# Performance work log

Hardware: AMD Instinct MI355X
Metric: run time of the kernel (lower is better)

## Reference

```python
import jax, jax.numpy as jnp
import numpy as np

N = 50000   # nodes
D = 256     # embed_dim
H = 256     # hidden_dim
E = 250000  # edges per relation type
T = 3       # edge types
NEG_SLOPE = 0.2  # PyG GATConv default


def setup_inputs() -> dict:
    key = jax.random.key(0)
    ks = jax.random.split(key, 12)
    s = lambda k, shape: jax.random.normal(k, shape, jnp.float32) * 0.05
    z = jax.random.normal(ks[0], (N, D), jnp.float32)
    ei = jax.random.randint(ks[1], (T, 2, E), 0, N, dtype=jnp.int32)
    W1 = s(ks[2], (T, D, H)); as1 = s(ks[3], (T, H)); ad1 = s(ks[4], (T, H))
    b1 = jnp.zeros((T, H), jnp.float32)
    W2 = s(ks[5], (T, H, H)); as2 = s(ks[6], (T, H)); ad2 = s(ks[7], (T, H))
    b2 = jnp.zeros((T, H), jnp.float32)
    Wh = s(ks[8], (H, 1)); bh = jnp.zeros((1,), jnp.float32)
    return dict(z=z, ei=ei, W1=W1, as1=as1, ad1=ad1, b1=b1,
                W2=W2, as2=as2, ad2=ad2, b2=b2, Wh=Wh, bh=bh)


def gat_conv(x, ei, W, a_s, a_d, b):
    # PyG GATConv, heads=1, no self loops: h = x W; e_ij = leaky_relu(a_s.h_j + a_d.h_i)
    # alpha = softmax over incoming edges of node i; out_i = sum_j alpha_ij h_j + bias
    src, dst = ei[0], ei[1]
    n = x.shape[0]
    h = x @ W                              # [N, H]
    a_src = h @ a_s                        # [N]
    a_dst = h @ a_d                        # [N]
    e = jax.nn.leaky_relu(a_src[src] + a_dst[dst], NEG_SLOPE)   # [E]
    m = jax.ops.segment_max(e, dst, num_segments=n)             # per-dst max
    ex = jnp.exp(e - m[dst])
    den = jax.ops.segment_sum(ex, dst, num_segments=n)
    alpha = ex / den[dst]                                       # [E]
    out = jax.ops.segment_sum(h[src] * alpha[:, None], dst, num_segments=n)
    return out + b


def layer(x, ei, W, a_s, a_d, b):
    # sum of per-type GATConv outputs, then ReLU (matches module)
    outs = jax.vmap(lambda e_, W_, s_, d_, b_: gat_conv(x, e_, W_, s_, d_, b_))(ei, W, a_s, a_d, b)
    return jax.nn.relu(outs.sum(0))


def reference(z, ei, W1, as1, ad1, b1, W2, as2, ad2, b2, Wh, bh):
    h1 = layer(z, ei, W1, as1, ad1, b1)
    h2 = layer(h1, ei, W2, as2, ad2, b2)
    return jax.nn.sigmoid(h2 @ Wh + bh).squeeze(-1)   # [N]
```

## Files before the change

### kernel.cpp

```cpp
#include <hip/hip_runtime.h>

#define GAT_N 50000
#define GAT_D 256
#define GAT_T 3
#define GAT_E 250000
#define GAT_B (GAT_T*GAT_N)
#define GAT_TOTE (GAT_T*GAT_E)
#define GAT_COLS (GAT_T*GAT_D)
#define GAT_SLOPE 0.2f

typedef unsigned short u16;
typedef unsigned int u32;
typedef __attribute__((ext_vector_type(8))) short s16x8;
typedef __attribute__((ext_vector_type(8))) __bf16 bf16x8;
typedef __attribute__((ext_vector_type(4))) float f32x4;
typedef __attribute__((ext_vector_type(2))) u32 u32x2;

__device__ __forceinline__ u16 f2bf(float f) {
    u32 x = __builtin_bit_cast(u32, f);
    u32 r = (x + 0x7fffu + ((x >> 16) & 1u)) >> 16;
    return (u16)r;
}
__device__ __forceinline__ float lo16(u32 w) {
    return __builtin_bit_cast(float, w << 16);
}
__device__ __forceinline__ float hi16(u32 w) {
    return __builtin_bit_cast(float, w & 0xffff0000u);
}

template<int CTRL>
__device__ __forceinline__ float dppadd(float x) {
    int y = __builtin_amdgcn_update_dpp(0, __builtin_bit_cast(int, x),
                                        CTRL, 0xf, 0xf, true);
    return x + __builtin_bit_cast(float, y);
}
__device__ __forceinline__ float sum16(float x) {
    x = dppadd<0xB1>(x);
    x = dppadd<0x4E>(x);
    x = dppadd<0x141>(x);
    x = dppadd<0x140>(x);
    return x;
}

__global__ void gat_prep(const float* __restrict__ W1, const float* __restrict__ W2,
                         const float* __restrict__ z, const float* __restrict__ b1,
                         const float* __restrict__ b2, const int* __restrict__ ei,
                         u16* __restrict__ WT1b, u16* __restrict__ WT2b,
                         u16* __restrict__ zb, u32* __restrict__ deg,
                         int* __restrict__ psrc2, float* __restrict__ bias3)
{
    int idx = blockIdx.x * 256 + threadIdx.x;
    if (idx < GAT_T * GAT_D * GAT_D) {
        int t = idx >> 16, r = idx & 65535;
        int h = r >> 8, d = r & 255;
        WT1b[idx] = f2bf(W1[t * 65536 + d * 256 + h]);
        WT2b[idx] = f2bf(W2[t * 65536 + d * 256 + h]);
    }
    if (idx < 2 * GAT_D) {
        const float* bb = (idx < GAT_D) ? b1 : b2;
        int c = idx & 255;
        bias3[idx] = bb[c] + bb[GAT_D + c] + bb[2 * GAT_D + c];
    }
    if (idx < GAT_TOTE) {
        int t = idx / GAT_E;
        int e = idx - t * GAT_E;
        int src = ei[t * 2 * GAT_E + e];
        int dst = ei[t * 2 * GAT_E + GAT_E + e];
        u32 slot = atomicAdd(&deg[dst], 1u);
        if (slot < 64u)
            psrc2[(size_t)dst * 64 + slot] = t * GAT_N + src;
    }
    if (idx < GAT_N * GAT_D / 4) {
        f32x4 v = ((const f32x4*)z)[idx];
        ushort4 pk;
        pk.x = f2bf(v.x); pk.y = f2bf(v.y); pk.z = f2bf(v.z); pk.w = f2bf(v.w);
        ((ushort4*)zb)[idx] = pk;
    }
}

__global__ __launch_bounds__(512, 4) void gat_gemm(
    const u16* __restrict__ A, const u16* __restrict__ WTb,
    u16* __restrict__ H, const float* __restrict__ as_in,
    const float* __restrict__ ad_in, float* __restrict__ a_s,
    float* __restrict__ a_d)
{
    int lin = blockIdx.x;
    int g   = lin / 48;
    int rem = lin - g * 48;
    int bc  = rem >> 3;
    int br  = (g << 3) + (rem & 7);
    if (br >= 391) return;

    __shared__ u16 Als[2][128 * 64];
    __shared__ u16 Bls[2][128 * 64];
    int tid  = threadIdx.x;
    int wave = tid >> 6, lane = tid & 63;
    int quad = lane >> 4, l16 = lane & 15;
    int wm = wave & 1, wn = wave >> 1;
    int lrow = lane >> 3;
    int swz  = ((lane & 7) ^ lrow) * 8;

    size_t arow0 = (size_t)br * 128;
    size_t brow0 = (size_t)bc * 128;

    auto STAGE = [&](int buf, int ks) {
        int k0 = ks * 64;
        #pragma unroll
        for (int r = 0; r < 2; ++r) {
            int srow = wave * 16 + r * 8 + lrow;
            const u16* gA = A   + (arow0 + srow) * GAT_D + k0 + swz;
            const u16* gB = WTb + (brow0 + srow) * GAT_D + k0 + swz;
            u16* lA = &Als[buf][wave * 1024 + r * 512];
            u16* lB = &Bls[buf][wave * 1024 + r * 512];
#if defined(__has_builtin) && __has_builtin(__builtin_amdgcn_global_load_lds)
            __builtin_amdgcn_global_load_lds(
                (const __attribute__((address_space(1))) void*)gA,
                (__attribute__((address_space(3))) void*)lA, 16, 0, 0);
            __builtin_amdgcn_global_load_lds(
                (const __attribute__((address_space(1))) void*)gB,
                (__attribute__((address_space(3))) void*)lB, 16, 0, 0);
#else
            *(s16x8*)(lA + lane * 8) = *(const s16x8*)gA;
            *(s16x8*)(lB + lane * 8) = *(const s16x8*)gB;
#endif
        }
    };

    f32x4 acc[4][2] = {};

    STAGE(0, 0);
    #pragma unroll
    for (int ks = 0; ks < 4; ++ks) {
        int cur = ks & 1;
        if (ks < 3) {
            STAGE(cur ^ 1, ks + 1);
            asm volatile("s_waitcnt vmcnt(4)" ::: "memory");
        } else {
            asm volatile("s_waitcnt vmcnt(0)" ::: "memory");
        }
        __builtin_amdgcn_s_barrier();

        #pragma unroll
        for (int kk = 0; kk < 2; ++kk) {
            int csw8 = ((kk * 4 + quad) ^ (l16 & 7)) * 8;
            bf16x8 af[4], bf[2];
            #pragma unroll
            for (int i = 0; i < 4; ++i)
                af[i] = __builtin_bit_cast(bf16x8,
                    *(const s16x8*)(&Als[cur][(wm * 64 + i * 16 + l16) * 64 + csw8]));
            #pragma unroll
            for (int j = 0; j < 2; ++j)
                bf[j] = __builtin_bit_cast(bf16x8,
                    *(const s16x8*)(&Bls[cur][(wn * 32 + j * 16 + l16) * 64 + csw8]));
            #pragma unroll
            for (int i = 0; i < 4; ++i)
                #pragma unroll
                for (int j = 0; j < 2; ++j)
                    acc[i][j] = __builtin_amdgcn_mfma_f32_16x16x32_bf16(
                        af[i], bf[j], acc[i][j], 0, 0, 0);
        }
        if (ks < 3)
            __builtin_amdgcn_s_barrier();
    }

    int gcol0 = bc * 128 + wn * 32;
    int t   = gcol0 >> 8;
    int ch0 = gcol0 & 255;
    u16* Ht = H + (size_t)t * GAT_N * GAT_D;
    int rowb = br * 128 + wm * 64 + quad * 4;
    #pragma unroll
    for (int i = 0; i < 4; ++i) {
        #pragma unroll
        for (int j = 0; j < 2; ++j) {
            int ch = ch0 + j * 16 + l16;
            #pragma unroll
            for (int r = 0; r < 4; ++r) {
                int row = rowb + i * 16 + r;
                if (row < GAT_N) Ht[(size_t)row * GAT_D + ch] = f2bf(acc[i][j][r]);
            }
        }
    }

    float asv[2], adv[2];
    #pragma unroll
    for (int j = 0; j < 2; ++j) {
        int ch = ch0 + j * 16 + l16;
        asv[j] = as_in[t * GAT_D + ch];
        adv[j] = ad_in[t * GAT_D + ch];
    }
    #pragma unroll
    for (int i = 0; i < 4; ++i) {
        float ps[4] = {}, pd[4] = {};
        #pragma unroll
        for (int j = 0; j < 2; ++j) {
            f32x4 a = acc[i][j];
            #pragma unroll
            for (int r = 0; r < 4; ++r) {
                ps[r] += a[r] * asv[j];
                pd[r] += a[r] * adv[j];
            }
        }
        #pragma unroll
        for (int r = 0; r < 4; ++r) {
            ps[r] = sum16(ps[r]);
            pd[r] = sum16(pd[r]);
        }
        if (l16 == 0) {
            int row = rowb + i * 16;
            #pragma unroll
            for (int r = 0; r < 4; ++r) {
                if (row + r < GAT_N) {
                    atomicAdd(&a_s[t * GAT_N + row + r], ps[r]);
                    atomicAdd(&a_d[t * GAT_N + row + r], pd[r]);
                }
            }
        }
    }
}

__global__ __launch_bounds__(64) void gat_gather(
    const u32* __restrict__ deg, const int* __restrict__ psrc2,
    const float* __restrict__ a_src, const float* __restrict__ a_dst,
    const u16* __restrict__ Hfb, const float* __restrict__ bias3,
    const float* __restrict__ Wh, const float* __restrict__ bh,
    int layer, u16* __restrict__ x2b, float* __restrict__ out)
{
    int n = blockIdx.x;
    int lane = threadIdx.x;

    u32 dv = deg[n];
    int dtot = (dv > 64u) ? 64 : (int)dv;

    int  j     = lane;
    bool valid = j < dtot;
    int  rs    = valid ? psrc2[(size_t)n * 64 + j] : 0;
    int  tj    = (rs >= GAT_N) + (rs >= 2 * GAT_N);

    float as   = a_src[rs];
    float adn  = a_dst[tj * GAT_N + n];

    const u16* Hl = Hfb + lane * 4;
    u32x2 w[8];
    #pragma unroll
    for (int u = 0; u < 8; ++u) {
        int rv = __builtin_amdgcn_readlane(rs, u);
        w[u] = *(const u32x2*)(Hl + (size_t)rv * GAT_D);
    }

    float e = as + adn;
    e = (e > 0.f) ? e : GAT_SLOPE * e;
    float ex = valid ? __expf(e) : 0.f;

    float s0 = (tj == 0) ? ex : 0.f;
    float s1 = (tj == 1) ? ex : 0.f;
    float s2 = (tj == 2) ? ex : 0.f;
    s0 = sum16(s0); s1 = sum16(s1); s2 = sum16(s2);
    #pragma unroll
    for (int d = 16; d < 64; d <<= 1) {
        s0 += __shfl_xor(s0, d);
        s1 += __shfl_xor(s1, d);
        s2 += __shfl_xor(s2, d);
    }
    float den = (tj == 0) ? s0 : ((tj == 1) ? s1 : s2);
    float alv = valid ? ex / den : 0.f;
    int av = __builtin_bit_cast(int, alv);

    float r[4] = {};
    int dpad = (dtot + 7) & ~7;
    for (int k0 = 0; ; k0 += 8) {
        float al[8]; u32x2 wc[8];
        #pragma unroll
        for (int u = 0; u < 8; ++u) {
            wc[u] = w[u];
            al[u] = __builtin_bit_cast(float,
                        __builtin_amdgcn_readlane(av, k0 + u));
        }
        bool more = (k0 + 8 < dpad);
        if (more) {
            #pragma unroll
            for (int u = 0; u < 8; ++u) {
                int rv = __builtin_amdgcn_readlane(rs, k0 + 8 + u);
                w[u] = *(const u32x2*)(Hl + (size_t)rv * GAT_D);
            }
        }
        #pragma unroll
        for (int u = 0; u < 8; ++u) {
            r[0] += al[u] * lo16(wc[u].x);
            r[1] += al[u] * hi16(wc[u].x);
            r[2] += al[u] * lo16(wc[u].y);
            r[3] += al[u] * hi16(wc[u].y);
        }
        if (!more) break;
    }

    int c0 = lane * 4;
    const float* b3 = bias3 + layer * GAT_D;
    float v[4];
    #pragma unroll
    for (int i = 0; i < 4; ++i) v[i] = fmaxf(r[i] + b3[c0 + i], 0.f);

    if (layer == 0) {
        u16 pk[4];
        #pragma unroll
        for (int i = 0; i < 4; ++i) pk[i] = f2bf(v[i]);
        *(ushort4*)(x2b + (size_t)n * GAT_D + c0) = *(ushort4*)pk;
    } else {
        float wsum = 0.f;
        #pragma unroll
        for (int i = 0; i < 4; ++i) wsum += v[i] * Wh[c0 + i];
        wsum = sum16(wsum);
        wsum += __shfl_xor(wsum, 16);
        wsum += __shfl_xor(wsum, 32);
        if (lane == 0) out[n] = 1.0f / (1.0f + __expf(-(wsum + bh[0])));
    }
}

__global__ void PyGTypeSpecificGAT_80075370266775_kernel() {}

extern "C" void kernel_launch(void* const* d_in, const int* in_sizes, int n_in,
                              void* d_out, int out_size, void* d_ws, size_t ws_size,
                              hipStream_t stream)
{
    (void)in_sizes; (void)n_in; (void)out_size; (void)ws_size;
    const float* z   = (const float*)d_in[0];
    const int*   ei  = (const int*)d_in[1];
    const float* W1  = (const float*)d_in[2];
    const float* as1 = (const float*)d_in[3];
    const float* ad1 = (const float*)d_in[4];
    const float* b1  = (const float*)d_in[5];
    const float* W2  = (const float*)d_in[6];
    const float* as2 = (const float*)d_in[7];
    const float* ad2 = (const float*)d_in[8];
    const float* b2  = (const float*)d_in[9];
    const float* Wh  = (const float*)d_in[10];
    const float* bh  = (const float*)d_in[11];
    float* out = (float*)d_out;

    char* p = (char*)d_ws;
    u16*  Hfb  = (u16*)p;  p += (size_t)GAT_T * GAT_N * GAT_D * 2;
    u16*  x2b  = (u16*)p;  p += (size_t)GAT_N * GAT_D * 2;
    u16*  zb   = (u16*)p;  p += (size_t)GAT_N * GAT_D * 2;
    char* zero_base = p;
    u32*  deg  = (u32*)p;  p += (size_t)GAT_N * 4;
    float* a0s = (float*)p; p += (size_t)GAT_B * 4;
    float* a0d = (float*)p; p += (size_t)GAT_B * 4;
    float* a1s = (float*)p; p += (size_t)GAT_B * 4;
    float* a1d = (float*)p; p += (size_t)GAT_B * 4;
    size_t zbytes = (size_t)(p - zero_base);
    int*  psrc2 = (int*)p; p += (size_t)GAT_N * 64 * 4;
    u16*  WT1b = (u16*)p;  p += (size_t)GAT_COLS * GAT_D * 2;
    u16*  WT2b = (u16*)p;  p += (size_t)GAT_COLS * GAT_D * 2;
    float* bias3 = (float*)p; p += 2 * GAT_D * 4;

    const int PREP_BLKS = (GAT_N * GAT_D / 4 + 255) / 256;

    hipMemsetAsync(zero_base, 0, zbytes, stream);
    gat_prep<<<PREP_BLKS, 256, 0, stream>>>(W1, W2, z, b1, b2, ei,
                                            WT1b, WT2b, zb, deg, psrc2,
                                            bias3);

    const int GEMM_BLKS = 49 * 48;

    for (int layer = 0; layer < 2; ++layer) {
        const u16*   A   = (layer == 0) ? zb   : x2b;
        const u16*   WTb = (layer == 0) ? WT1b : WT2b;
        const float* as_ = (layer == 0) ? as1  : as2;
        const float* ad_ = (layer == 0) ? ad1  : ad2;
        float* aS = (layer == 0) ? a0s : a1s;
        float* aD = (layer == 0) ? a0d : a1d;

        gat_gemm<<<GEMM_BLKS, 512, 0, stream>>>(A, WTb, Hfb, as_, ad_,
                                                aS, aD);
        gat_gather<<<GAT_N, 64, 0, stream>>>(deg, psrc2, aS, aD,
                                             Hfb, bias3, Wh, bh,
                                             layer, x2b, out);
    }
}
```

Before: 381.4 us.

## Widen GEMM tile to full edge-type columns and reduce attention scores in LDS

Each GEMM block now computes a 128x256 tile covering all channels of one edge type, using 1024 threads and a larger B staging buffer. Because the whole row sits in one block, the attention-score dot products are reduced through shared memory and written directly, which removes the global float atomics. That also removes the need to zero the score buffers, so one shared pair of score arrays replaces the per-layer pairs. The cost is higher LDS use (about 104 KB per block) and a tighter register budget under the new launch bounds, which can lower occupancy or cause spills.

```diff
diff --git a/kernel.cpp b/kernel.cpp
--- a/kernel.cpp
+++ b/kernel.cpp
@@ -78,21 +78,30 @@
     }
 }
 
-__global__ __launch_bounds__(512, 4) void gat_gemm(
+__global__ __launch_bounds__(1024, 4) void gat_gemm(
     const u16* __restrict__ A, const u16* __restrict__ WTb,
     u16* __restrict__ H, const float* __restrict__ as_in,
     const float* __restrict__ ad_in, float* __restrict__ a_s,
     float* __restrict__ a_d)
 {
     int lin = blockIdx.x;
-    int g   = lin / 48;
-    int rem = lin - g * 48;
-    int bc  = rem >> 3;
-    int br  = (g << 3) + (rem & 7);
-    if (br >= 391) return;
+    int br, t;
+    if (lin < 1152) {
+        int q = lin / 24, rem = lin - q * 24;
+        t  = rem >> 3;
+        br = (q << 3) + (rem & 7);
+    } else {
+        int idx = lin - 1152;
+        int gi = idx / 3;
+        br = 384 + gi;
+        t  = idx - gi * 3;
+    }
 
     __shared__ u16 Als[2][128 * 64];
-    __shared__ u16 Bls[2][128 * 64];
+    __shared__ u16 Bls[2][256 * 64];
+    __shared__ float reds[8][128];
+    __shared__ float redd[8][128];
+
     int tid  = threadIdx.x;
     int wave = tid >> 6, lane = tid & 63;
     int quad = lane >> 4, l16 = lane & 15;
@@ -101,26 +110,32 @@
     int swz  = ((lane & 7) ^ lrow) * 8;
 
     size_t arow0 = (size_t)br * 128;
-    size_t brow0 = (size_t)bc * 128;
+    size_t brow0 = (size_t)t  * 256;
 
     auto STAGE = [&](int buf, int ks) {
         int k0 = ks * 64;
-        #pragma unroll
-        for (int r = 0; r < 2; ++r) {
-            int srow = wave * 16 + r * 8 + lrow;
-            const u16* gA = A   + (arow0 + srow) * GAT_D + k0 + swz;
-            const u16* gB = WTb + (brow0 + srow) * GAT_D + k0 + swz;
-            u16* lA = &Als[buf][wave * 1024 + r * 512];
-            u16* lB = &Bls[buf][wave * 1024 + r * 512];
+        {
+            int srow = wave * 8 + lrow;
+            const u16* gA = A + (arow0 + srow) * GAT_D + k0 + swz;
+            u16* lA = &Als[buf][wave * 512];
 #if defined(__has_builtin) && __has_builtin(__builtin_amdgcn_global_load_lds)
             __builtin_amdgcn_global_load_lds(
                 (const __attribute__((address_space(1))) void*)gA,
                 (__attribute__((address_space(3))) void*)lA, 16, 0, 0);
+#else
+            *(s16x8*)(lA + lane * 8) = *(const s16x8*)gA;
+#endif
+        }
+        #pragma unroll
+        for (int r = 0; r < 2; ++r) {
+            int srow = wave * 16 + r * 8 + lrow;
+            const u16* gB = WTb + (brow0 + srow) * GAT_D + k0 + swz;
+            u16* lB = &Bls[buf][wave * 1024 + r * 512];
+#if defined(__has_builtin) && __has_builtin(__builtin_amdgcn_global_load_lds)
             __builtin_amdgcn_global_load_lds(
                 (const __attribute__((address_space(1))) void*)gB,
                 (__attribute__((address_space(3))) void*)lB, 16, 0, 0);
 #else
-            *(s16x8*)(lA + lane * 8) = *(const s16x8*)gA;
             *(s16x8*)(lB + lane * 8) = *(const s16x8*)gB;
 #endif
         }
@@ -134,7 +149,7 @@
         int cur = ks & 1;
         if (ks < 3) {
             STAGE(cur ^ 1, ks + 1);
-            asm volatile("s_waitcnt vmcnt(4)" ::: "memory");
+            asm volatile("s_waitcnt vmcnt(3)" ::: "memory");
         } else {
             asm volatile("s_waitcnt vmcnt(0)" ::: "memory");
         }
@@ -163,9 +178,7 @@
             __builtin_amdgcn_s_barrier();
     }
 
-    int gcol0 = bc * 128 + wn * 32;
-    int t   = gcol0 >> 8;
-    int ch0 = gcol0 & 255;
+    int ch0 = wn * 32;
     u16* Ht = H + (size_t)t * GAT_N * GAT_D;
     int rowb = br * 128 + wm * 64 + quad * 4;
     #pragma unroll
@@ -206,13 +219,29 @@
             pd[r] = sum16(pd[r]);
         }
         if (l16 == 0) {
-            int row = rowb + i * 16;
+            int rl = wm * 64 + i * 16 + quad * 4;
             #pragma unroll
             for (int r = 0; r < 4; ++r) {
-                if (row + r < GAT_N) {
-                    atomicAdd(&a_s[t * GAT_N + row + r], ps[r]);
-                    atomicAdd(&a_d[t * GAT_N + row + r], pd[r]);
-                }
+                reds[wn][rl + r] = ps[r];
+                redd[wn][rl + r] = pd[r];
+            }
+        }
+    }
+    __syncthreads();
+    if (tid < 256) {
+        int row = tid & 127;
+        int grow = br * 128 + row;
+        if (grow < GAT_N) {
+            if (tid < 128) {
+                float s = 0.f;
+                #pragma unroll
+                for (int w = 0; w < 8; ++w) s += reds[w][row];
+                a_s[t * GAT_N + grow] = s;
+            } else {
+                float s = 0.f;
+                #pragma unroll
+                for (int w = 0; w < 8; ++w) s += redd[w][row];
+                a_d[t * GAT_N + grow] = s;
             }
         }
     }
@@ -340,38 +369,31 @@
     u16*  Hfb  = (u16*)p;  p += (size_t)GAT_T * GAT_N * GAT_D * 2;
     u16*  x2b  = (u16*)p;  p += (size_t)GAT_N * GAT_D * 2;
     u16*  zb   = (u16*)p;  p += (size_t)GAT_N * GAT_D * 2;
-    char* zero_base = p;
+    float* a_src = (float*)p; p += (size_t)GAT_B * 4;
+    float* a_dst = (float*)p; p += (size_t)GAT_B * 4;
     u32*  deg  = (u32*)p;  p += (size_t)GAT_N * 4;
-    float* a0s = (float*)p; p += (size_t)GAT_B * 4;
-    float* a0d = (float*)p; p += (size_t)GAT_B * 4;
-    float* a1s = (float*)p; p += (size_t)GAT_B * 4;
-    float* a1d = (float*)p; p += (size_t)GAT_B * 4;
-    size_t zbytes = (size_t)(p - zero_base);
     int*  psrc2 = (int*)p; p += (size_t)GAT_N * 64 * 4;
     u16*  WT1b = (u16*)p;  p += (size_t)GAT_COLS * GAT_D * 2;
     u16*  WT2b = (u16*)p;  p += (size_t)GAT_COLS * GAT_D * 2;
     float* bias3 = (float*)p; p += 2 * GAT_D * 4;
 
     const int PREP_BLKS = (GAT_N * GAT_D / 4 + 255) / 256;
-
-    hipMemsetAsync(zero_base, 0, zbytes, stream);
+    const int GEMM_BLKS = 1173;
+
+    hipMemsetAsync(deg, 0, (size_t)GAT_N * 4, stream);
     gat_prep<<<PREP_BLKS, 256, 0, stream>>>(W1, W2, z, b1, b2, ei,
                                             WT1b, WT2b, zb, deg, psrc2,
                                             bias3);
-
-    const int GEMM_BLKS = 49 * 48;
 
     for (int layer = 0; layer < 2; ++layer) {
         const u16*   A   = (layer == 0) ? zb   : x2b;
         const u16*   WTb = (layer == 0) ? WT1b : WT2b;
         const float* as_ = (layer == 0) ? as1  : as2;
         const float* ad_ = (layer == 0) ? ad1  : ad2;
-        float* aS = (layer == 0) ? a0s : a1s;
-        float* aD = (layer == 0) ? a0d : a1d;
-
-        gat_gemm<<<GEMM_BLKS, 512, 0, stream>>>(A, WTb, Hfb, as_, ad_,
-                                                aS, aD);
-        gat_gather<<<GAT_N, 64, 0, stream>>>(deg, psrc2, aS, aD,
+
+        gat_gemm<<<GEMM_BLKS, 1024, 0, stream>>>(A, WTb, Hfb, as_, ad_,
+                                                 a_src, a_dst);
+        gat_gather<<<GAT_N, 64, 0, stream>>>(deg, psrc2, a_src, a_dst,
                                              Hfb, bias3, Wh, bh,
                                              layer, x2b, out);
     }
```

After: 356.3 us. -6.6%, faster.
